# Optimization experiments

Measured on AMD Instinct MI355X. Metric: run time of the kernel, lower is better.

Reference implementation:

```python
import jax, jax.numpy as jnp
import numpy as np

B, N, E, H = 32, 512, 256, 8
HD = E // H
EPS = 1e-5

def setup_inputs() -> dict:
    key = jax.random.key(0)
    ks = jax.random.split(key, 10)
    x = jax.random.normal(ks[0], (B, N, E), dtype=jnp.float32)
    # boolean masks: True = masked out. Keep diagonal unmasked so no row is fully masked.
    pre = jax.random.bernoulli(ks[1], 0.1, (B, H, N, N))
    eye = jnp.eye(N, dtype=bool)
    pre_mask = jnp.where(eye[None, None, :, :], False, pre)
    post_attn_mask = jax.random.bernoulli(ks[2], 0.1, (B, N))
    s = 1.0 / np.sqrt(E)
    in_proj_w = jax.random.uniform(ks[3], (3 * E, E), jnp.float32, -s, s)
    in_proj_b = jnp.zeros((3 * E,), jnp.float32)
    out_w = jax.random.uniform(ks[4], (E, E), jnp.float32, -s, s)
    out_b = jnp.zeros((E,), jnp.float32)
    gamma = jnp.ones((E,), jnp.float32)
    beta = jnp.zeros((E,), jnp.float32)
    return {"x": x, "pre_mask": pre_mask, "post_attn_mask": post_attn_mask,
            "in_proj_w": in_proj_w, "in_proj_b": in_proj_b,
            "out_w": out_w, "out_b": out_b, "gamma": gamma, "beta": beta}

def reference(x, pre_mask, post_attn_mask, in_proj_w, in_proj_b, out_w, out_b, gamma, beta):
    b, n, e = x.shape
    # fused qkv projection (matches nn.MultiheadAttention in_proj)
    qkv = x @ in_proj_w.T + in_proj_b            # [B,N,3E]
    q, k, v = jnp.split(qkv, 3, axis=-1)
    def heads(t):
        return t.reshape(b, n, H, HD).transpose(0, 2, 1, 3)  # [B,H,N,HD]
    q, k, v = heads(q), heads(k), heads(v)
    scores = jnp.einsum('bhqd,bhkd->bhqk', q * (HD ** -0.5), k)  # [B,H,N,N]
    scores = jnp.where(pre_mask, -1e9, scores)
    w = jax.nn.softmax(scores, axis=-1)                          # [B,H,N,N]
    o = jnp.einsum('bhqk,bhkd->bhqd', w, v)                      # [B,H,N,HD]
    o = o.transpose(0, 2, 1, 3).reshape(b, n, e)
    o = o @ out_w.T + out_b
    # post-attention mask: zero outputs of unavailable agents
    o = jnp.where(post_attn_mask[:, :, None], 0.0, o)
    # residual + LayerNorm
    y = x + o
    mu = y.mean(axis=-1, keepdims=True)
    var = y.var(axis=-1, keepdims=True)
    out = (y - mu) * jax.lax.rsqrt(var + EPS) * gamma + beta
    # attn_weights averaged over heads (PyTorch default average_attn_weights=True)
    attn_weights = w.mean(axis=1)                                # [B,N,N]
    return (out, attn_weights)
```

## Files before the change

kernel.cpp:

```cpp
#include <hip/hip_runtime.h>

#define BB 32
#define NN 512
#define EE 256
#define HH 8
#define HDD 32

typedef __attribute__((ext_vector_type(4))) float f32x4;
typedef __attribute__((ext_vector_type(8))) short s16x8;
typedef unsigned short ushort_t;
typedef unsigned int uint_t;

__device__ __forceinline__ ushort_t f2bf(float f) {
  union { float f; uint_t u; } v; v.f = f;
  uint_t r = v.u + 0x7fffu + ((v.u >> 16) & 1u);
  return (ushort_t)(r >> 16);
}

__global__ __launch_bounds__(256) void qkv_kernel(
    const float* __restrict__ x, const float* __restrict__ w,
    const float* __restrict__ bias,
    ushort_t* __restrict__ Q, ushort_t* __restrict__ K, ushort_t* __restrict__ V) {
  __shared__ float As[16][68];
  __shared__ float Bs[16][68];
  int t = threadIdx.x;
  int bx = blockIdx.x % 12;
  int by = blockIdx.x / 12;
  int m0 = by * 64, j0 = bx * 64;
  int tx = t & 15, ty = t >> 4;
  float4 c4[4];
  #pragma unroll
  for (int i = 0; i < 4; i++) { c4[i].x = 0.f; c4[i].y = 0.f; c4[i].z = 0.f; c4[i].w = 0.f; }
  int skk = t & 15, sbase = t >> 4;
  for (int kc = 0; kc < 256; kc += 16) {
    __syncthreads();
    #pragma unroll
    for (int i = 0; i < 4; i++) {
      int mm = sbase + 16 * i;
      As[skk][mm] = x[(m0 + mm) * 256 + kc + skk];
      Bs[skk][mm] = w[(j0 + mm) * 256 + kc + skk];
    }
    __syncthreads();
    #pragma unroll
    for (int k2 = 0; k2 < 16; k2++) {
      float4 bv = *(const float4*)&Bs[k2][tx * 4];
      #pragma unroll
      for (int i = 0; i < 4; i++) {
        float a = As[k2][ty * 4 + i];
        c4[i].x += a * bv.x; c4[i].y += a * bv.y; c4[i].z += a * bv.z; c4[i].w += a * bv.w;
      }
    }
  }
  int j = j0 + tx * 4;
  int which = j >> 8;
  int e0 = j & 255;
  int h = e0 >> 5, d0 = e0 & 31;
  ushort_t* dst = (which == 0) ? Q : ((which == 1) ? K : V);
  float4 b4 = *(const float4*)&bias[j];
  #pragma unroll
  for (int i = 0; i < 4; i++) {
    int m = m0 + ty * 4 + i;
    int bi = m >> 9, n = m & 511;
    float fx = c4[i].x + b4.x, fy = c4[i].y + b4.y, fz = c4[i].z + b4.z, fw = c4[i].w + b4.w;
    uint_t lo = (uint_t)f2bf(fx) | ((uint_t)f2bf(fy) << 16);
    uint_t hi = (uint_t)f2bf(fz) | ((uint_t)f2bf(fw) << 16);
    uint2 pk; pk.x = lo; pk.y = hi;
    *(uint2*)&dst[(((size_t)(bi * 8 + h) * 512 + n) * 32) + d0] = pk;
  }
}

__global__ __launch_bounds__(256) void attn_kernel(
    const ushort_t* __restrict__ Q, const ushort_t* __restrict__ K,
    const ushort_t* __restrict__ V, const int* __restrict__ pre_mask,
    float* __restrict__ o, float* __restrict__ attnw) {
  __shared__ ushort_t sQ[16 * 32];
  __shared__ ushort_t sP[16 * 520];
  __shared__ float sSum[4][16];
  __shared__ float sO[4][16 * 32];

  int t = threadIdx.x;
  int bb = blockIdx.x >> 5;
  int q0 = (blockIdx.x & 31) << 4;
  int w = t >> 6;
  int lane = t & 63;
  int quad = lane >> 4;
  int l16 = lane & 15;
  int kbase = w * 128;
  const float scale = 0.17677669529663687f;

  float wmean[4][8];
  #pragma unroll
  for (int i = 0; i < 4; i++)
    #pragma unroll
    for (int j = 0; j < 8; j++) wmean[i][j] = 0.f;

  for (int h = 0; h < 8; h++) {
    size_t base = ((size_t)(bb * 8 + h) * 512) * 32;
    const ushort_t* Kg = K + base;
    const ushort_t* Vg = V + base;
    const int* mbase = pre_mask + ((size_t)(bb * 8 + h) * 512 + q0) * 512;

    if (t < 64) {
      ((s16x8*)sQ)[t] = ((const s16x8*)(Q + base + (size_t)q0 * 32))[t];
    }
    __syncthreads();

    s16x8 afrag = *(const s16x8*)&sQ[l16 * 32 + quad * 8];
    float ev[8][4];
    #pragma unroll
    for (int t8 = 0; t8 < 8; t8++) {
      int n0 = kbase + t8 * 16;
      s16x8 bfrag = *(const s16x8*)&Kg[(size_t)(n0 + l16) * 32 + quad * 8];
      f32x4 acc = {0.f, 0.f, 0.f, 0.f};
      acc = __builtin_amdgcn_mfma_f32_16x16x32_bf16(afrag, bfrag, acc, 0, 0, 0);
      #pragma unroll
      for (int i = 0; i < 4; i++) {
        int msk = mbase[(quad * 4 + i) * 512 + n0 + l16];
        ev[t8][i] = msk ? 0.f : __expf(acc[i] * scale);
      }
    }
    float ps[4];
    #pragma unroll
    for (int i = 0; i < 4; i++) {
      float s = 0.f;
      #pragma unroll
      for (int t8 = 0; t8 < 8; t8++) s += ev[t8][i];
      s += __shfl_xor(s, 1, 64);
      s += __shfl_xor(s, 2, 64);
      s += __shfl_xor(s, 4, 64);
      s += __shfl_xor(s, 8, 64);
      ps[i] = s;
    }
    if (l16 == 0) {
      #pragma unroll
      for (int i = 0; i < 4; i++) sSum[w][quad * 4 + i] = ps[i];
    }
    #pragma unroll
    for (int t8 = 0; t8 < 8; t8++)
      #pragma unroll
      for (int i = 0; i < 4; i++)
        sP[(quad * 4 + i) * 520 + kbase + t8 * 16 + l16] = f2bf(ev[t8][i]);
    __syncthreads();

    float inv[4];
    #pragma unroll
    for (int i = 0; i < 4; i++) {
      int r = quad * 4 + i;
      inv[i] = 1.0f / (sSum[0][r] + sSum[1][r] + sSum[2][r] + sSum[3][r]);
    }
    #pragma unroll
    for (int t8 = 0; t8 < 8; t8++)
      #pragma unroll
      for (int i = 0; i < 4; i++)
        wmean[i][t8] += 0.125f * ev[t8][i] * inv[i];

    f32x4 oacc[2];
    oacc[0] = (f32x4){0.f, 0.f, 0.f, 0.f};
    oacc[1] = (f32x4){0.f, 0.f, 0.f, 0.f};
    #pragma unroll
    for (int ks = 0; ks < 4; ks++) {
      s16x8 pa = *(const s16x8*)&sP[l16 * 520 + kbase + ks * 32 + quad * 8];
      #pragma unroll
      for (int dt = 0; dt < 2; dt++) {
        s16x8 vb;
        #pragma unroll
        for (int j = 0; j < 8; j++)
          vb[j] = (short)Vg[(size_t)(kbase + ks * 32 + quad * 8 + j) * 32 + dt * 16 + l16];
        oacc[dt] = __builtin_amdgcn_mfma_f32_16x16x32_bf16(pa, vb, oacc[dt], 0, 0, 0);
      }
    }
    #pragma unroll
    for (int dt = 0; dt < 2; dt++)
      #pragma unroll
      for (int i = 0; i < 4; i++)
        sO[w][(quad * 4 + i) * 32 + dt * 16 + l16] = oacc[dt][i];
    __syncthreads();

    {
      int r = t >> 4;
      int c = (t & 15) * 2;
      float s0 = sO[0][r * 32 + c] + sO[1][r * 32 + c] + sO[2][r * 32 + c] + sO[3][r * 32 + c];
      float s1 = sO[0][r * 32 + c + 1] + sO[1][r * 32 + c + 1] + sO[2][r * 32 + c + 1] + sO[3][r * 32 + c + 1];
      float invr = 1.0f / (sSum[0][r] + sSum[1][r] + sSum[2][r] + sSum[3][r]);
      float2 ov; ov.x = s0 * invr; ov.y = s1 * invr;
      *(float2*)&o[((size_t)(bb * 512 + q0 + r) * 256) + h * 32 + c] = ov;
    }
  }

  float* arow = attnw + (size_t)(bb * 512 + q0) * 512;
  #pragma unroll
  for (int i = 0; i < 4; i++)
    #pragma unroll
    for (int t8 = 0; t8 < 8; t8++)
      arow[(quad * 4 + i) * 512 + kbase + t8 * 16 + l16] = wmean[i][t8];
}

__global__ __launch_bounds__(256) void proj_ln_kernel(
    const float* __restrict__ x, const float* __restrict__ w,
    const float* __restrict__ bias, const int* __restrict__ post_mask,
    const float* __restrict__ gamma, const float* __restrict__ beta,
    float* __restrict__ io ) {
  __shared__ float As[16][17];
  __shared__ float Bs[16][260];
  int t = threadIdx.x;
  int m0 = blockIdx.x * 16;
  int tx = t & 63, ty = t >> 6;
  float4 c4[4];
  #pragma unroll
  for (int i = 0; i < 4; i++) { c4[i].x = 0.f; c4[i].y = 0.f; c4[i].z = 0.f; c4[i].w = 0.f; }
  int skk = t & 15, srr = t >> 4;
  for (int kc = 0; kc < 256; kc += 16) {
    __syncthreads();
    As[skk][srr] = io[(m0 + srr) * 256 + kc + skk];
    #pragma unroll
    for (int i = 0; i < 16; i++) {
      int idx = t + i * 256;
      int kk = idx & 15, jj = idx >> 4;
      Bs[kk][jj] = w[jj * 256 + kc + kk];
    }
    __syncthreads();
    #pragma unroll
    for (int k2 = 0; k2 < 16; k2++) {
      float4 bv = *(const float4*)&Bs[k2][tx * 4];
      #pragma unroll
      for (int i = 0; i < 4; i++) {
        float a = As[k2][ty * 4 + i];
        c4[i].x += a * bv.x; c4[i].y += a * bv.y; c4[i].z += a * bv.z; c4[i].w += a * bv.w;
      }
    }
  }
  int j0 = tx * 4;
  float4 gm = *(const float4*)&gamma[j0];
  float4 bt = *(const float4*)&beta[j0];
  float4 ob = *(const float4*)&bias[j0];
  float4 yv[4];
  float s1[4], s2[4];
  #pragma unroll
  for (int i = 0; i < 4; i++) {
    int m = m0 + ty * 4 + i;
    int bi = m >> 9, n = m & 511;
    bool msk = post_mask[bi * 512 + n] != 0;
    float4 xv = *(const float4*)&x[m * 256 + j0];
    float4 pv;
    pv.x = msk ? 0.f : c4[i].x + ob.x;
    pv.y = msk ? 0.f : c4[i].y + ob.y;
    pv.z = msk ? 0.f : c4[i].z + ob.z;
    pv.w = msk ? 0.f : c4[i].w + ob.w;
    float4 y;
    y.x = xv.x + pv.x; y.y = xv.y + pv.y; y.z = xv.z + pv.z; y.w = xv.w + pv.w;
    yv[i] = y;
    s1[i] = y.x + y.y + y.z + y.w;
    s2[i] = y.x * y.x + y.y * y.y + y.z * y.z + y.w * y.w;
  }
  #pragma unroll
  for (int off = 32; off > 0; off >>= 1) {
    #pragma unroll
    for (int i = 0; i < 4; i++) {
      s1[i] += __shfl_xor(s1[i], off, 64);
      s2[i] += __shfl_xor(s2[i], off, 64);
    }
  }
  #pragma unroll
  for (int i = 0; i < 4; i++) {
    int m = m0 + ty * 4 + i;
    float mu = s1[i] * (1.0f / 256.0f);
    float var = s2[i] * (1.0f / 256.0f) - mu * mu;
    float rstd = rsqrtf(var + 1e-5f);
    float4 y = yv[i];
    float4 outv;
    outv.x = (y.x - mu) * rstd * gm.x + bt.x;
    outv.y = (y.y - mu) * rstd * gm.y + bt.y;
    outv.z = (y.z - mu) * rstd * gm.z + bt.z;
    outv.w = (y.w - mu) * rstd * gm.w + bt.w;
    *(float4*)&io[m * 256 + j0] = outv;
  }
}

extern "C" void kernel_launch(void* const* d_in, const int* in_sizes, int n_in,
                              void* d_out, int out_size, void* d_ws, size_t ws_size,
                              hipStream_t stream) {
  const float* x       = (const float*)d_in[0];
  const int*   pre_m   = (const int*)d_in[1];
  const int*   post_m  = (const int*)d_in[2];
  const float* in_w    = (const float*)d_in[3];
  const float* in_b    = (const float*)d_in[4];
  const float* out_w   = (const float*)d_in[5];
  const float* out_b   = (const float*)d_in[6];
  const float* gamma   = (const float*)d_in[7];
  const float* beta    = (const float*)d_in[8];
  float* out   = (float*)d_out;
  float* attnw = out + (size_t)BB * NN * EE;
  ushort_t* Q = (ushort_t*)d_ws;
  ushort_t* K = Q + (size_t)BB * HH * NN * HDD;
  ushort_t* V = K + (size_t)BB * HH * NN * HDD;

  qkv_kernel<<<dim3(3072), dim3(256), 0, stream>>>(x, in_w, in_b, Q, K, V);
  attn_kernel<<<dim3(1024), dim3(256), 0, stream>>>(Q, K, V, pre_m, out, attnw);
  proj_ln_kernel<<<dim3(1024), dim3(256), 0, stream>>>(x, out_w, out_b, post_m, gamma, beta, out);
}
```

Baseline: 544.2 us.

## Use bf16 MFMA for QKV and output projections with bf16 attention output

```diff
diff --git a/kernel.cpp b/kernel.cpp
--- a/kernel.cpp
+++ b/kernel.cpp
@@ -16,63 +16,75 @@
   uint_t r = v.u + 0x7fffu + ((v.u >> 16) & 1u);
   return (ushort_t)(r >> 16);
 }
-
-__global__ __launch_bounds__(256) void qkv_kernel(
+__device__ __forceinline__ uint_t pk2(float a, float b) {
+  return (uint_t)f2bf(a) | ((uint_t)f2bf(b) << 16);
+}
+
+__global__ __launch_bounds__(256) void qkv_mfma(
     const float* __restrict__ x, const float* __restrict__ w,
     const float* __restrict__ bias,
     ushort_t* __restrict__ Q, ushort_t* __restrict__ K, ushort_t* __restrict__ V) {
-  __shared__ float As[16][68];
-  __shared__ float Bs[16][68];
+  __shared__ ushort_t sA[128][40];
+  __shared__ ushort_t sB[128][40];
   int t = threadIdx.x;
-  int bx = blockIdx.x % 12;
-  int by = blockIdx.x / 12;
-  int m0 = by * 64, j0 = bx * 64;
-  int tx = t & 15, ty = t >> 4;
-  float4 c4[4];
-  #pragma unroll
-  for (int i = 0; i < 4; i++) { c4[i].x = 0.f; c4[i].y = 0.f; c4[i].z = 0.f; c4[i].w = 0.f; }
-  int skk = t & 15, sbase = t >> 4;
-  for (int kc = 0; kc < 256; kc += 16) {
+  int bj = blockIdx.x % 6, bm = blockIdx.x / 6;
+  int m0 = bm * 128, j0 = bj * 128;
+  int w4 = t >> 6, lane = t & 63, quad = lane >> 4, l16 = lane & 15;
+  int wy = w4 >> 1, wx = w4 & 1;
+  f32x4 acc[4][4];
+  #pragma unroll
+  for (int a = 0; a < 4; a++)
+    #pragma unroll
+    for (int b = 0; b < 4; b++) acc[a][b] = (f32x4){0.f, 0.f, 0.f, 0.f};
+  int sr = t >> 3, sc = t & 7;
+  for (int kk = 0; kk < 256; kk += 32) {
     __syncthreads();
     #pragma unroll
     for (int i = 0; i < 4; i++) {
-      int mm = sbase + 16 * i;
-      As[skk][mm] = x[(m0 + mm) * 256 + kc + skk];
-      Bs[skk][mm] = w[(j0 + mm) * 256 + kc + skk];
-    }
-    __syncthreads();
-    #pragma unroll
-    for (int k2 = 0; k2 < 16; k2++) {
-      float4 bv = *(const float4*)&Bs[k2][tx * 4];
-      #pragma unroll
-      for (int i = 0; i < 4; i++) {
-        float a = As[k2][ty * 4 + i];
-        c4[i].x += a * bv.x; c4[i].y += a * bv.y; c4[i].z += a * bv.z; c4[i].w += a * bv.w;
+      int r = sr + 32 * i;
+      float4 av = *(const float4*)&x[(size_t)(m0 + r) * 256 + kk + sc * 4];
+      float4 bv = *(const float4*)&w[(size_t)(j0 + r) * 256 + kk + sc * 4];
+      uint2 pa; pa.x = pk2(av.x, av.y); pa.y = pk2(av.z, av.w);
+      uint2 pb; pb.x = pk2(bv.x, bv.y); pb.y = pk2(bv.z, bv.w);
+      *(uint2*)&sA[r][sc * 4] = pa;
+      *(uint2*)&sB[r][sc * 4] = pb;
+    }
+    __syncthreads();
+    s16x8 af[4], bf[4];
+    #pragma unroll
+    for (int mt = 0; mt < 4; mt++)
+      af[mt] = *(const s16x8*)&sA[wy * 64 + mt * 16 + l16][quad * 8];
+    #pragma unroll
+    for (int jt = 0; jt < 4; jt++)
+      bf[jt] = *(const s16x8*)&sB[wx * 64 + jt * 16 + l16][quad * 8];
+    #pragma unroll
+    for (int mt = 0; mt < 4; mt++)
+      #pragma unroll
+      for (int jt = 0; jt < 4; jt++)
+        acc[mt][jt] = __builtin_amdgcn_mfma_f32_16x16x32_bf16(af[mt], bf[jt], acc[mt][jt], 0, 0, 0);
+  }
+  #pragma unroll
+  for (int jt = 0; jt < 4; jt++) {
+    int j = j0 + wx * 64 + jt * 16 + l16;
+    int which = j >> 8, e0 = j & 255, h = e0 >> 5, d0 = e0 & 31;
+    ushort_t* dst = (which == 0) ? Q : ((which == 1) ? K : V);
+    float b = bias[j];
+    #pragma unroll
+    for (int mt = 0; mt < 4; mt++) {
+      #pragma unroll
+      for (int r = 0; r < 4; r++) {
+        int m = m0 + wy * 64 + mt * 16 + quad * 4 + r;
+        int bi = m >> 9, n = m & 511;
+        dst[((size_t)(bi * 8 + h) * 512 + n) * 32 + d0] = f2bf(acc[mt][jt][r] + b);
       }
     }
-  }
-  int j = j0 + tx * 4;
-  int which = j >> 8;
-  int e0 = j & 255;
-  int h = e0 >> 5, d0 = e0 & 31;
-  ushort_t* dst = (which == 0) ? Q : ((which == 1) ? K : V);
-  float4 b4 = *(const float4*)&bias[j];
-  #pragma unroll
-  for (int i = 0; i < 4; i++) {
-    int m = m0 + ty * 4 + i;
-    int bi = m >> 9, n = m & 511;
-    float fx = c4[i].x + b4.x, fy = c4[i].y + b4.y, fz = c4[i].z + b4.z, fw = c4[i].w + b4.w;
-    uint_t lo = (uint_t)f2bf(fx) | ((uint_t)f2bf(fy) << 16);
-    uint_t hi = (uint_t)f2bf(fz) | ((uint_t)f2bf(fw) << 16);
-    uint2 pk; pk.x = lo; pk.y = hi;
-    *(uint2*)&dst[(((size_t)(bi * 8 + h) * 512 + n) * 32) + d0] = pk;
   }
 }
 
 __global__ __launch_bounds__(256) void attn_kernel(
     const ushort_t* __restrict__ Q, const ushort_t* __restrict__ K,
     const ushort_t* __restrict__ V, const int* __restrict__ pre_mask,
-    float* __restrict__ o, float* __restrict__ attnw) {
+    ushort_t* __restrict__ O, float* __restrict__ attnw) {
   __shared__ ushort_t sQ[16 * 32];
   __shared__ ushort_t sP[16 * 520];
   __shared__ float sSum[4][16];
@@ -182,8 +194,8 @@
       float s0 = sO[0][r * 32 + c] + sO[1][r * 32 + c] + sO[2][r * 32 + c] + sO[3][r * 32 + c];
       float s1 = sO[0][r * 32 + c + 1] + sO[1][r * 32 + c + 1] + sO[2][r * 32 + c + 1] + sO[3][r * 32 + c + 1];
       float invr = 1.0f / (sSum[0][r] + sSum[1][r] + sSum[2][r] + sSum[3][r]);
-      float2 ov; ov.x = s0 * invr; ov.y = s1 * invr;
-      *(float2*)&o[((size_t)(bb * 512 + q0 + r) * 256) + h * 32 + c] = ov;
+      uint_t pk = pk2(s0 * invr, s1 * invr);
+      *(uint_t*)&O[((size_t)(bb * 512 + q0 + r) * 256) + h * 32 + c] = pk;
     }
   }
 
@@ -195,84 +207,64 @@
       arow[(quad * 4 + i) * 512 + kbase + t8 * 16 + l16] = wmean[i][t8];
 }
 
-__global__ __launch_bounds__(256) void proj_ln_kernel(
-    const float* __restrict__ x, const float* __restrict__ w,
-    const float* __restrict__ bias, const int* __restrict__ post_mask,
+__global__ __launch_bounds__(256) void proj_ln_mfma(
+    const ushort_t* __restrict__ O, const float* __restrict__ x,
+    const float* __restrict__ w, const float* __restrict__ bias,
+    const int* __restrict__ post_mask,
     const float* __restrict__ gamma, const float* __restrict__ beta,
-    float* __restrict__ io ) {
-  __shared__ float As[16][17];
-  __shared__ float Bs[16][260];
+    float* __restrict__ out) {
+  __shared__ ushort_t sB[256][40];
   int t = threadIdx.x;
-  int m0 = blockIdx.x * 16;
-  int tx = t & 63, ty = t >> 6;
-  float4 c4[4];
-  #pragma unroll
-  for (int i = 0; i < 4; i++) { c4[i].x = 0.f; c4[i].y = 0.f; c4[i].z = 0.f; c4[i].w = 0.f; }
-  int skk = t & 15, srr = t >> 4;
-  for (int kc = 0; kc < 256; kc += 16) {
-    __syncthreads();
-    As[skk][srr] = io[(m0 + srr) * 256 + kc + skk];
-    #pragma unroll
-    for (int i = 0; i < 16; i++) {
-      int idx = t + i * 256;
-      int kk = idx & 15, jj = idx >> 4;
-      Bs[kk][jj] = w[jj * 256 + kc + kk];
-    }
-    __syncthreads();
-    #pragma unroll
-    for (int k2 = 0; k2 < 16; k2++) {
-      float4 bv = *(const float4*)&Bs[k2][tx * 4];
-      #pragma unroll
-      for (int i = 0; i < 4; i++) {
-        float a = As[k2][ty * 4 + i];
-        c4[i].x += a * bv.x; c4[i].y += a * bv.y; c4[i].z += a * bv.z; c4[i].w += a * bv.w;
-      }
-    }
-  }
-  int j0 = tx * 4;
-  float4 gm = *(const float4*)&gamma[j0];
-  float4 bt = *(const float4*)&beta[j0];
-  float4 ob = *(const float4*)&bias[j0];
-  float4 yv[4];
-  float s1[4], s2[4];
+  int m0 = blockIdx.x * 64;
+  int w4 = t >> 6, lane = t & 63, quad = lane >> 4, l16 = lane & 15;
+  int mrow0 = m0 + w4 * 16;
+  f32x4 acc[16];
+  #pragma unroll
+  for (int jt = 0; jt < 16; jt++) acc[jt] = (f32x4){0.f, 0.f, 0.f, 0.f};
+  int sr = t >> 3, sc = t & 7;
+  for (int kk = 0; kk < 256; kk += 32) {
+    __syncthreads();
+    #pragma unroll
+    for (int i = 0; i < 8; i++) {
+      int r = sr + 32 * i;
+      float4 bv = *(const float4*)&w[(size_t)r * 256 + kk + sc * 4];
+      uint2 pb; pb.x = pk2(bv.x, bv.y); pb.y = pk2(bv.z, bv.w);
+      *(uint2*)&sB[r][sc * 4] = pb;
+    }
+    __syncthreads();
+    s16x8 af = *(const s16x8*)&O[(size_t)(mrow0 + l16) * 256 + kk + quad * 8];
+    #pragma unroll
+    for (int jt = 0; jt < 16; jt++) {
+      s16x8 bf = *(const s16x8*)&sB[jt * 16 + l16][quad * 8];
+      acc[jt] = __builtin_amdgcn_mfma_f32_16x16x32_bf16(af, bf, acc[jt], 0, 0, 0);
+    }
+  }
   #pragma unroll
   for (int i = 0; i < 4; i++) {
-    int m = m0 + ty * 4 + i;
+    int m = mrow0 + quad * 4 + i;
     int bi = m >> 9, n = m & 511;
     bool msk = post_mask[bi * 512 + n] != 0;
-    float4 xv = *(const float4*)&x[m * 256 + j0];
-    float4 pv;
-    pv.x = msk ? 0.f : c4[i].x + ob.x;
-    pv.y = msk ? 0.f : c4[i].y + ob.y;
-    pv.z = msk ? 0.f : c4[i].z + ob.z;
-    pv.w = msk ? 0.f : c4[i].w + ob.w;
-    float4 y;
-    y.x = xv.x + pv.x; y.y = xv.y + pv.y; y.z = xv.z + pv.z; y.w = xv.w + pv.w;
-    yv[i] = y;
-    s1[i] = y.x + y.y + y.z + y.w;
-    s2[i] = y.x * y.x + y.y * y.y + y.z * y.z + y.w * y.w;
-  }
-  #pragma unroll
-  for (int off = 32; off > 0; off >>= 1) {
-    #pragma unroll
-    for (int i = 0; i < 4; i++) {
-      s1[i] += __shfl_xor(s1[i], off, 64);
-      s2[i] += __shfl_xor(s2[i], off, 64);
-    }
-  }
-  #pragma unroll
-  for (int i = 0; i < 4; i++) {
-    int m = m0 + ty * 4 + i;
-    float mu = s1[i] * (1.0f / 256.0f);
-    float var = s2[i] * (1.0f / 256.0f) - mu * mu;
+    float y[16];
+    float s1 = 0.f, s2 = 0.f;
+    #pragma unroll
+    for (int jt = 0; jt < 16; jt++) {
+      int j = jt * 16 + l16;
+      float p = msk ? 0.f : (acc[jt][i] + bias[j]);
+      float yy = x[(size_t)m * 256 + j] + p;
+      y[jt] = yy; s1 += yy; s2 += yy * yy;
+    }
+    s1 += __shfl_xor(s1, 1, 64); s1 += __shfl_xor(s1, 2, 64);
+    s1 += __shfl_xor(s1, 4, 64); s1 += __shfl_xor(s1, 8, 64);
+    s2 += __shfl_xor(s2, 1, 64); s2 += __shfl_xor(s2, 2, 64);
+    s2 += __shfl_xor(s2, 4, 64); s2 += __shfl_xor(s2, 8, 64);
+    float mu = s1 * (1.0f / 256.0f);
+    float var = s2 * (1.0f / 256.0f) - mu * mu;
     float rstd = rsqrtf(var + 1e-5f);
-    float4 y = yv[i];
-    float4 outv;
-    outv.x = (y.x - mu) * rstd * gm.x + bt.x;
-    outv.y = (y.y - mu) * rstd * gm.y + bt.y;
-    outv.z = (y.z - mu) * rstd * gm.z + bt.z;
-    outv.w = (y.w - mu) * rstd * gm.w + bt.w;
-    *(float4*)&io[m * 256 + j0] = outv;
+    #pragma unroll
+    for (int jt = 0; jt < 16; jt++) {
+      int j = jt * 16 + l16;
+      out[(size_t)m * 256 + j] = (y[jt] - mu) * rstd * gamma[j] + beta[j];
+    }
   }
 }
 
@@ -293,8 +285,9 @@
   ushort_t* Q = (ushort_t*)d_ws;
   ushort_t* K = Q + (size_t)BB * HH * NN * HDD;
   ushort_t* V = K + (size_t)BB * HH * NN * HDD;
-
-  qkv_kernel<<<dim3(3072), dim3(256), 0, stream>>>(x, in_w, in_b, Q, K, V);
-  attn_kernel<<<dim3(1024), dim3(256), 0, stream>>>(Q, K, V, pre_m, out, attnw);
-  proj_ln_kernel<<<dim3(1024), dim3(256), 0, stream>>>(x, out_w, out_b, post_m, gamma, beta, out);
-}
+  ushort_t* O = V + (size_t)BB * HH * NN * HDD;
+
+  qkv_mfma<<<dim3(768), dim3(256), 0, stream>>>(x, in_w, in_b, Q, K, V);
+  attn_kernel<<<dim3(1024), dim3(256), 0, stream>>>(Q, K, V, pre_m, O, attnw);
+  proj_ln_mfma<<<dim3(256), dim3(256), 0, stream>>>(O, x, out_w, out_b, post_m, gamma, beta, out);
+}
```

Result: faster. 503.6 us (-7.5%).
